# Kernel optimization log

Hardware: AMD Instinct MI355X
Metric: run time of the kernel (lower is better)

Reference implementation:

```python
import jax, jax.numpy as jnp
import numpy as np

D_MODEL = 256
D_EDGE = 64
EPS = 1e-05
INPUT_FEATS = 2 * D_MODEL + D_EDGE + 1  # 577


def _linear_params(key, fan_in, fan_out):
    k1, k2 = jax.random.split(key)
    lim = 1.0 / np.sqrt(fan_in)
    W = jax.random.uniform(k1, (fan_in, fan_out), minval=-lim, maxval=lim, dtype=jnp.float32)
    b = jax.random.uniform(k2, (fan_out,), minval=-lim, maxval=lim, dtype=jnp.float32)
    return W, b


def setup_inputs() -> dict:
    key = jax.random.key(0)
    ks = jax.random.split(key, 16)
    B, N = 8, 128
    inp = {
        "coords": jax.random.normal(ks[0], (B, N, 3), dtype=jnp.float32),
        "inv_feats": jax.random.normal(ks[1], (B, N, D_MODEL), dtype=jnp.float32),
        "adj_matrix": jnp.ones((B, N, N), dtype=jnp.float32),
        "atom_mask": jnp.ones((B, N), dtype=jnp.float32),
        "edge_feats": jax.random.normal(ks[2], (B, N, N, D_EDGE), dtype=jnp.float32),
    }
    inp["W_e1"], inp["b_e1"] = _linear_params(ks[3], INPUT_FEATS, D_MODEL)
    inp["W_e2"], inp["b_e2"] = _linear_params(ks[4], D_MODEL, D_MODEL)
    inp["W_att"], inp["b_att"] = _linear_params(ks[5], D_MODEL, 1)
    inp["W_h1"], inp["b_h1"] = _linear_params(ks[6], 2 * D_MODEL, D_MODEL)
    inp["W_h2"], inp["b_h2"] = _linear_params(ks[7], D_MODEL, D_MODEL)
    inp["W_x1"], inp["b_x1"] = _linear_params(ks[8], INPUT_FEATS, D_MODEL)
    inp["W_x2"], inp["b_x2"] = _linear_params(ks[9], D_MODEL, D_MODEL)
    inp["W_x3"], inp["b_x3"] = _linear_params(ks[10], D_MODEL, 1)
    return inp


def _pair_linear(W, b, node_feats, ef):
    # Linear over concat([node_i, node_j, ef]) without materializing the concat.
    # W: [2*d_model + d_edge + 1, out]
    d = D_MODEL
    hi = node_feats @ W[:d]          # [B,N,out]
    hj = node_feats @ W[d:2 * d]     # [B,N,out]
    he = ef @ W[2 * d:]              # [B,N,N,out]
    return hi[:, :, None, :] + hj[:, None, :, :] + he + b


def _egnn_forward(coords, inv_feats, adj_matrix, atom_mask, edge_feats,
                  W_e1, b_e1, W_e2, b_e2, W_att, b_att,
                  W_h1, b_h1, W_h2, b_h2, W_x1, b_x1, W_x2, b_x2, W_x3, b_x3):
    mask = atom_mask[..., None]                       # [B,N,1]
    diff = coords[:, :, None, :] - coords[:, None, :, :]   # [B,N,N,3]
    sq = jnp.sum(diff * diff, axis=-1, keepdims=True)      # [B,N,N,1]
    ef = jnp.concatenate([edge_feats, sq], axis=-1)        # [B,N,N,d_edge+1]
    adj = adj_matrix[..., None]                             # [B,N,N,1]

    # phi_e: Linear-SiLU-Linear-SiLU on pair features
    msg = jax.nn.silu(_pair_linear(W_e1, b_e1, inv_feats, ef))
    msg = jax.nn.silu(msg @ W_e2 + b_e2)                    # [B,N,N,d]

    att = jax.nn.sigmoid(msg @ W_att + b_att)               # [B,N,N,1]
    node_msg = jnp.sum(msg * att * adj, axis=2)             # [B,N,d]

    h = jnp.concatenate([inv_feats, node_msg], axis=-1)
    h = jax.nn.silu(h @ W_h1 + b_h1) @ W_h2 + b_h2          # [B,N,d]

    # phi_x: Linear-SiLU-Linear-SiLU-Linear -> scalar per edge
    ex = jax.nn.silu(_pair_linear(W_x1, b_x1, inv_feats, ef))
    ex = jax.nn.silu(ex @ W_x2 + b_x2)
    edge_attn = ex @ W_x3 + b_x3                             # [B,N,N,1]

    normalisers = jnp.sqrt(sq[..., 0] + EPS) + 1.0           # [B,N,N]
    weighted = diff * edge_attn / normalisers[..., None] * adj
    coord_updates = jnp.sum(weighted, axis=2)                # [B,N,3]
    num_nodes = jnp.sum(mask, axis=1) + 1.0                  # [B,1]
    coord_updates = coord_updates / num_nodes[:, :, None]

    out_coords = (coords + coord_updates) * mask
    out_feats = h * mask
    return out_coords, out_feats


def reference(coords, inv_feats, adj_matrix, atom_mask, edge_feats,
              W_e1, b_e1, W_e2, b_e2, W_att, b_att,
              W_h1, b_h1, W_h2, b_h2, W_x1, b_x1, W_x2, b_x2, W_x3, b_x3):
    return _egnn_forward(coords, inv_feats, adj_matrix, atom_mask, edge_feats,
                         W_e1, b_e1, W_e2, b_e2, W_att, b_att,
                         W_h1, b_h1, W_h2, b_h2, W_x1, b_x1, W_x2, b_x2, W_x3, b_x3)
```

## Files before the change

kernel.cpp:

```cpp
#include <hip/hip_runtime.h>

typedef __attribute__((ext_vector_type(8))) __bf16 bf16x8;
typedef __attribute__((ext_vector_type(4))) __bf16 bf16x4;
typedef __attribute__((ext_vector_type(4))) float f32x4;

__device__ __forceinline__ float fast_sig(float x) {
  return __builtin_amdgcn_rcpf(1.0f + __expf(-x));
}
__device__ __forceinline__ float siluf(float x) { return x * fast_sig(x); }
__device__ __forceinline__ __bf16 tobf(float x) { return (__bf16)x; }

__global__ __launch_bounds__(256) void k_prep(
    const float* __restrict__ We1, const float* __restrict__ Wx1,
    const float* __restrict__ We2, const float* __restrict__ Wx2,
    const float* __restrict__ Wh1, const float* __restrict__ Wh2,
    const float* __restrict__ invf,
    __bf16* __restrict__ wt_e, __bf16* __restrict__ wt_x,
    __bf16* __restrict__ w2e, __bf16* __restrict__ w2x,
    __bf16* __restrict__ wh1t, __bf16* __restrict__ wh2t,
    __bf16* __restrict__ invb,
    float* __restrict__ nmsg, float* __restrict__ cupd)
{
  int idx = blockIdx.x * 256 + threadIdx.x;
  if (idx < 147456) {
    int kk = idx / 576, f = idx - kk * 576;
    wt_e[idx] = tobf(We1[f * 256 + kk]);
    wt_x[idx] = tobf(Wx1[f * 256 + kk]);
  }
  if (idx < 65536) {
    int c = idx >> 8, k = idx & 255;
    w2e[idx] = tobf(We2[k * 256 + c]);
    w2x[idx] = tobf(Wx2[k * 256 + c]);
    wh2t[idx] = tobf(Wh2[k * 256 + c]);
    f32x4 z = {0.f, 0.f, 0.f, 0.f};
    *(f32x4*)(nmsg + idx * 4) = z;
  }
  if (idx < 131072) {
    int c = idx >> 9, k = idx & 511;
    wh1t[idx] = tobf(Wh1[k * 256 + c]);
  }
  if (idx < 3072) cupd[idx] = 0.f;
  invb[idx] = tobf(invf[idx]);
}

template<int NKS>
__device__ __forceinline__ void node_gemm64(
    const __bf16* __restrict__ B, int ldb, int boff,
    const __bf16* __restrict__ A, int lda, int aoff,
    int row0, int tid, f32x4 acc[4][4])
{
  const int lane = tid & 63, wc = tid >> 6, lr = lane & 15, lg = lane >> 4;
  #pragma unroll
  for (int ks = 0; ks < NKS; ks++) {
    bf16x8 bB[4], aA[4];
    #pragma unroll
    for (int m = 0; m < 4; m++)
      bB[m] = *(const bf16x8*)(B + (size_t)(row0 + m * 16 + lr) * ldb + boff + ks * 32 + lg * 8);
    #pragma unroll
    for (int n = 0; n < 4; n++)
      aA[n] = *(const bf16x8*)(A + (size_t)(wc * 64 + n * 16 + lr) * lda + aoff + ks * 32 + lg * 8);
    #pragma unroll
    for (int m = 0; m < 4; m++)
      #pragma unroll
      for (int n = 0; n < 4; n++)
        acc[m][n] = __builtin_amdgcn_mfma_f32_16x16x32_bf16(aA[n], bB[m], acc[m][n], 0, 0, 0);
  }
}

__global__ __launch_bounds__(256) void k_nproj(
    const __bf16* __restrict__ invb,
    const __bf16* __restrict__ wt_e, const __bf16* __restrict__ wt_x,
    const float* __restrict__ be1, const float* __restrict__ bx1,
    float* __restrict__ hie, float* __restrict__ hix,
    __bf16* __restrict__ hje, __bf16* __restrict__ hjx)
{
  const int tid = threadIdx.x;
  const int row0 = blockIdx.x * 64;
  const int mat = blockIdx.y;
  const __bf16* A = (mat < 2) ? wt_e : wt_x;
  const int aoff = (mat & 1) ? 256 : 0;

  f32x4 acc[4][4];
  #pragma unroll
  for (int m = 0; m < 4; m++)
    #pragma unroll
    for (int n = 0; n < 4; n++) { f32x4 z = {0.f,0.f,0.f,0.f}; acc[m][n] = z; }
  node_gemm64<8>(invb, 256, 0, A, 576, aoff, row0, tid, acc);

  const int lane = tid & 63, wc = tid >> 6, lr = lane & 15, lg = lane >> 4;
  if ((mat & 1) == 0) {
    const float* bias = (mat == 0) ? be1 : bx1;
    float* out = (mat == 0) ? hie : hix;
    #pragma unroll
    for (int m = 0; m < 4; m++) {
      int node = row0 + m * 16 + lr;
      #pragma unroll
      for (int n = 0; n < 4; n++) {
        int c0 = wc * 64 + n * 16 + lg * 4;
        f32x4 v = acc[m][n] + *(const f32x4*)(bias + c0);
        *(f32x4*)(out + (size_t)node * 256 + c0) = v;
      }
    }
  } else {
    __bf16* out = (mat == 1) ? hje : hjx;
    #pragma unroll
    for (int m = 0; m < 4; m++) {
      int node = row0 + m * 16 + lr;
      #pragma unroll
      for (int n = 0; n < 4; n++) {
        int c0 = wc * 64 + n * 16 + lg * 4;
        bf16x4 pk;
        #pragma unroll
        for (int r = 0; r < 4; r++) pk[r] = tobf(acc[m][n][r]);
        *(bf16x4*)(out + (size_t)node * 256 + c0) = pk;
      }
    }
  }
}

__global__ __launch_bounds__(256) void k_h1(
    const __bf16* __restrict__ invb, const float* __restrict__ nmsg,
    const __bf16* __restrict__ wh1t,
    const float* __restrict__ bh1, __bf16* __restrict__ h1b)
{
  const int tid = threadIdx.x;
  const int row0 = blockIdx.x * 64;
  const int c0 = blockIdx.y * 64;
  const int lane = tid & 63, w = tid >> 6, lr = lane & 15, lg = lane >> 4;
  const int node = row0 + w * 16 + lr;

  f32x4 acc[4];
  #pragma unroll
  for (int n = 0; n < 4; n++) { f32x4 z = {0.f,0.f,0.f,0.f}; acc[n] = z; }

  #pragma unroll
  for (int ks = 0; ks < 16; ks++) {
    bf16x8 bB;
    if (ks < 8) {
      bB = *(const bf16x8*)(invb + (size_t)node * 256 + ks * 32 + lg * 8);
    } else {
      const float* pp = nmsg + (size_t)node * 256 + (ks - 8) * 32 + lg * 8;
      f32x4 lo = *(const f32x4*)pp;
      f32x4 hi = *(const f32x4*)(pp + 4);
      bf16x8 t;
      t[0]=tobf(lo[0]); t[1]=tobf(lo[1]); t[2]=tobf(lo[2]); t[3]=tobf(lo[3]);
      t[4]=tobf(hi[0]); t[5]=tobf(hi[1]); t[6]=tobf(hi[2]); t[7]=tobf(hi[3]);
      bB = t;
    }
    #pragma unroll
    for (int n = 0; n < 4; n++) {
      bf16x8 aA = *(const bf16x8*)(wh1t + (size_t)(c0 + n * 16 + lr) * 512 + ks * 32 + lg * 8);
      acc[n] = __builtin_amdgcn_mfma_f32_16x16x32_bf16(aA, bB, acc[n], 0, 0, 0);
    }
  }

  #pragma unroll
  for (int n = 0; n < 4; n++) {
    int cc = c0 + n * 16 + lg * 4;
    f32x4 b4 = *(const f32x4*)(bh1 + cc);
    bf16x4 pk;
    #pragma unroll
    for (int r = 0; r < 4; r++) pk[r] = tobf(siluf(acc[n][r] + b4[r]));
    *(bf16x4*)(h1b + (size_t)node * 256 + cc) = pk;
  }
}

__global__ __launch_bounds__(256) void k_h2(
    const __bf16* __restrict__ h1b, const __bf16* __restrict__ wh2t,
    const float* __restrict__ bh2, const float* __restrict__ amask,
    const float* __restrict__ coords, const float* __restrict__ cupd,
    float* __restrict__ out_feats, float* __restrict__ out_coords)
{
  __shared__ float sM[2];
  const int tid = threadIdx.x;
  const int row0 = blockIdx.x * 64;
  const int c0 = blockIdx.y * 64;
  const int b = row0 >> 7;
  const int lane = tid & 63, w = tid >> 6, lr = lane & 15, lg = lane >> 4;
  const int node = row0 + w * 16 + lr;

  f32x4 acc[4];
  #pragma unroll
  for (int n = 0; n < 4; n++) { f32x4 z = {0.f,0.f,0.f,0.f}; acc[n] = z; }

  #pragma unroll
  for (int ks = 0; ks < 8; ks++) {
    bf16x8 bB = *(const bf16x8*)(h1b + (size_t)node * 256 + ks * 32 + lg * 8);
    #pragma unroll
    for (int n = 0; n < 4; n++) {
      bf16x8 aA = *(const bf16x8*)(wh2t + (size_t)(c0 + n * 16 + lr) * 256 + ks * 32 + lg * 8);
      acc[n] = __builtin_amdgcn_mfma_f32_16x16x32_bf16(aA, bB, acc[n], 0, 0, 0);
    }
  }

  float msk = amask[node];
  #pragma unroll
  for (int n = 0; n < 4; n++) {
    int cc = c0 + n * 16 + lg * 4;
    f32x4 b4 = *(const f32x4*)(bh2 + cc);
    f32x4 v = (acc[n] + b4) * msk;
    *(f32x4*)(out_feats + (size_t)node * 256 + cc) = v;
  }

  if (blockIdx.y == 0) {
    if (tid < 128) {
      float v = amask[b * 128 + tid];
      #pragma unroll
      for (int off = 1; off < 64; off <<= 1) v += __shfl_xor(v, off);
      if ((tid & 63) == 0) sM[tid >> 6] = v;
    }
    __syncthreads();
    const float sNum = sM[0] + sM[1];
    if (tid < 192) {
      int nl = tid / 3, d = tid - nl * 3;
      int nd = row0 + nl;
      float upd = cupd[nd * 3 + d] / (sNum + 1.0f);
      out_coords[nd * 3 + d] = (coords[nd * 3 + d] + upd) * amask[nd];
    }
  }
}

__global__ __launch_bounds__(512, 2) void k_edge(
    const float* __restrict__ coords, const float* __restrict__ adjm,
    const float* __restrict__ ef,
    const float* __restrict__ We1, const float* __restrict__ Wx1,
    const float* __restrict__ batt,
    const float* __restrict__ be2, const float* __restrict__ bx2,
    const float* __restrict__ bx3,
    const float* __restrict__ Watt, const float* __restrict__ Wx3,
    const float* __restrict__ hie, const float* __restrict__ hix,
    const __bf16* __restrict__ hje, const __bf16* __restrict__ hjx,
    const __bf16* __restrict__ wt_e, const __bf16* __restrict__ wt_x,
    const __bf16* __restrict__ w2e, const __bf16* __restrict__ w2x,
    float* __restrict__ nmsg, float* __restrict__ cupd)
{
  __shared__ __align__(16) char sSb[64 * 512];
  __shared__ __align__(16) __bf16 sE[2][64 * 72];
  __shared__ float sqv[2][64], sAdj[2][64], sRed[2][64];

  const int tid = threadIdx.x;
  const int d = blockIdx.x;
  const int p = (d >> 3) & 1;
  const int widx = (d >> 4) * 8 + (d & 7);
  const int lane = tid & 63;
  const int wv = tid >> 6;
  const int lr = lane & 15, lg = lane >> 4;
  const int cg = wv * 32;

  const float* hi_mat = p ? hix : hie;
  const __bf16* hj_mat = p ? hjx : hje;
  const float b0 = p ? bx3[0] : batt[0];

  f32x4 bb[2], vv[2], sl[2];
  #pragma unroll
  for (int n = 0; n < 2; n++) {
    bb[n] = *(const f32x4*)((p ? bx2 : be2) + cg + n * 16 + lg * 4);
    vv[n] = *(const f32x4*)((p ? Wx3 : Watt) + cg + n * 16 + lg * 4);
    sl[n] = *(const f32x4*)(((p ? Wx1 : We1) + 576 * 256) + cg + n * 16 + lg * 4);
  }

  const __bf16* wt = p ? wt_x : wt_e;
  const __bf16* w2 = p ? w2x : w2e;
  bf16x8 aW1[2][2], aW2[8][2];
  #pragma unroll
  for (int ks = 0; ks < 2; ks++)
    #pragma unroll
    for (int n = 0; n < 2; n++)
      aW1[ks][n] = *(const bf16x8*)(wt + (size_t)(cg + n * 16 + lr) * 576 + 512 + ks * 32 + lg * 8);
  #pragma unroll
  for (int ks = 0; ks < 8; ks++)
    #pragma unroll
    for (int n = 0; n < 2; n++)
      aW2[ks][n] = *(const bf16x8*)(w2 + (size_t)(cg + n * 16 + lr) * 256 + ks * 32 + lg * 8);

  const int erow = tid >> 3;
  const int ecol = (tid & 7) * 8;

  {
    const int h = widx * 8;
    const int bi0 = h >> 1;
    const int jg00 = (bi0 >> 7) * 128;
    if (tid < 64) {
      sRed[0][tid] = 0.f;
      int jg = jg00 + tid;
      float dx = coords[bi0 * 3 + 0] - coords[jg * 3 + 0];
      float dy = coords[bi0 * 3 + 1] - coords[jg * 3 + 1];
      float dz = coords[bi0 * 3 + 2] - coords[jg * 3 + 2];
      sqv[0][tid] = dx * dx + dy * dy + dz * dz;
    } else if (tid < 128) {
      sAdj[0][tid - 64] = adjm[(size_t)bi0 * 128 + (tid - 64)];
    }
    const float* er = ef + (size_t)bi0 * 8192 + erow * 64 + ecol;
    f32x4 x = *(const f32x4*)er;
    f32x4 y = *(const f32x4*)(er + 4);
    bf16x8 e8;
    e8[0]=tobf(x[0]); e8[1]=tobf(x[1]); e8[2]=tobf(x[2]); e8[3]=tobf(x[3]);
    e8[4]=tobf(y[0]); e8[5]=tobf(y[1]); e8[6]=tobf(y[2]); e8[7]=tobf(y[3]);
    *(bf16x8*)(&sE[0][0] + erow * 72 + ecol) = e8;
  }
  __syncthreads();

  for (int t = 0; t < 8; ++t) {
    const int h = widx * 8 + t;
    const int bi = h >> 1;
    const int jg0 = (bi >> 7) * 128 + (h & 1) * 64;
    const int cur = t & 1;
    const __bf16* sEc = &sE[cur][0];

    f32x4 hi4[2];
    bf16x4 hj4[4][2];
    #pragma unroll
    for (int n = 0; n < 2; n++)
      hi4[n] = *(const f32x4*)(hi_mat + (size_t)bi * 256 + cg + n * 16 + lg * 4);
    #pragma unroll
    for (int m = 0; m < 4; m++)
      #pragma unroll
      for (int n = 0; n < 2; n++)
        hj4[m][n] = *(const bf16x4*)(hj_mat + (size_t)(jg0 + m * 16 + lr) * 256 + cg + n * 16 + lg * 4);

    f32x4 acc[4][2];
    #pragma unroll
    for (int m = 0; m < 4; m++)
      #pragma unroll
      for (int n = 0; n < 2; n++) { f32x4 z = {0.f,0.f,0.f,0.f}; acc[m][n] = z; }

    #pragma unroll
    for (int ks = 0; ks < 2; ks++) {
      bf16x8 bE[4];
      #pragma unroll
      for (int m = 0; m < 4; m++)
        bE[m] = *(const bf16x8*)(sEc + (m * 16 + lr) * 72 + ks * 32 + lg * 8);
      __builtin_amdgcn_s_setprio(1);
      #pragma unroll
      for (int m = 0; m < 4; m++)
        #pragma unroll
        for (int n = 0; n < 2; n++)
          acc[m][n] = __builtin_amdgcn_mfma_f32_16x16x32_bf16(aW1[ks][n], bE[m], acc[m][n], 0, 0, 0);
      __builtin_amdgcn_s_setprio(0);
    }

    #pragma unroll
    for (int m = 0; m < 4; m++) {
      const int jl = m * 16 + lr;
      const float sq = sqv[cur][jl];
      #pragma unroll
      for (int n = 0; n < 2; n++) {
        const int kk0 = cg + n * 16 + lg * 4;
        bf16x4 pk;
        #pragma unroll
        for (int r = 0; r < 4; r++) {
          float v = acc[m][n][r] + hi4[n][r] + (float)hj4[m][n][r] + sq * sl[n][r];
          pk[r] = tobf(siluf(v));
        }
        int off = (jl * 512 + kk0 * 2) ^ ((jl & 7) << 4);
        *(bf16x4*)(sSb + off) = pk;
        f32x4 z = {0.f, 0.f, 0.f, 0.f};
        acc[m][n] = z;
      }
    }
    __syncthreads();

    f32x4 ex, ey;
    float nx = 0.f, ny = 0.f, nz = 0.f, njx = 0.f, njy = 0.f, njz = 0.f, nadj = 0.f;
    int bi_n = 0, jg0_n = 0;
    if (t < 7) {
      const int hn = h + 1;
      bi_n = hn >> 1;
      jg0_n = (bi_n >> 7) * 128 + (hn & 1) * 64;
      const float* er = ef + ((size_t)bi_n * 128 + (hn & 1) * 64) * 64 + erow * 64 + ecol;
      ex = *(const f32x4*)er;
      ey = *(const f32x4*)(er + 4);
      if (tid < 64) {
        int jg = jg0_n + tid;
        nx = coords[bi_n * 3 + 0]; ny = coords[bi_n * 3 + 1]; nz = coords[bi_n * 3 + 2];
        njx = coords[jg * 3 + 0]; njy = coords[jg * 3 + 1]; njz = coords[jg * 3 + 2];
      } else if (tid < 128) {
        nadj = adjm[(size_t)bi_n * 128 + ((hn & 1) * 64) + (tid - 64)];
      }
    }

    #pragma unroll
    for (int ks = 0; ks < 8; ks++) {
      bf16x8 bS[4];
      #pragma unroll
      for (int m = 0; m < 4; m++) {
        const int jl = m * 16 + lr;
        int off = (jl * 512 + (ks * 32 + lg * 8) * 2) ^ ((jl & 7) << 4);
        bS[m] = *(const bf16x8*)(sSb + off);
      }
      __builtin_amdgcn_s_setprio(1);
      #pragma unroll
      for (int m = 0; m < 4; m++)
        #pragma unroll
        for (int n = 0; n < 2; n++)
          acc[m][n] = __builtin_amdgcn_mfma_f32_16x16x32_bf16(aW2[ks][n], bS[m], acc[m][n], 0, 0, 0);
      __builtin_amdgcn_s_setprio(0);
    }

    float pr[4] = {0.f, 0.f, 0.f, 0.f};
    #pragma unroll
    for (int n = 0; n < 2; n++) {
      #pragma unroll
      for (int m = 0; m < 4; m++)
        #pragma unroll
        for (int r = 0; r < 4; r++) {
          float s = siluf(acc[m][n][r] + bb[n][r]);
          acc[m][n][r] = s;
          pr[m] += s * vv[n][r];
        }
    }
    #pragma unroll
    for (int m = 0; m < 4; m++) {
      pr[m] += __shfl_xor(pr[m], 16);
      pr[m] += __shfl_xor(pr[m], 32);
    }
    if (lane < 16) {
      #pragma unroll
      for (int m = 0; m < 4; m++)
        atomicAdd(&sRed[cur][m * 16 + lr], pr[m]);
    }

    if (t < 7) {
      const int nxt = cur ^ 1;
      bf16x8 e8;
      e8[0]=tobf(ex[0]); e8[1]=tobf(ex[1]); e8[2]=tobf(ex[2]); e8[3]=tobf(ex[3]);
      e8[4]=tobf(ey[0]); e8[5]=tobf(ey[1]); e8[6]=tobf(ey[2]); e8[7]=tobf(ey[3]);
      *(bf16x8*)(&sE[nxt][0] + erow * 72 + ecol) = e8;
      if (tid < 64) {
        sRed[nxt][tid] = 0.f;
        float dx = nx - njx, dy = ny - njy, dz = nz - njz;
        sqv[nxt][tid] = dx * dx + dy * dy + dz * dz;
      } else if (tid < 128) {
        sAdj[nxt][tid - 64] = nadj;
      }
    }
    __syncthreads();

    if (p == 0) {
      float aw[4];
      #pragma unroll
      for (int m = 0; m < 4; m++)
        aw[m] = fast_sig(sRed[cur][m * 16 + lr] + b0) * sAdj[cur][m * 16 + lr];
      f32x4 q[2];
      #pragma unroll
      for (int n = 0; n < 2; n++) { f32x4 z = {0.f,0.f,0.f,0.f}; q[n] = z; }
      #pragma unroll
      for (int m = 0; m < 4; m++)
        #pragma unroll
        for (int n = 0; n < 2; n++)
          q[n] += acc[m][n] * aw[m];
      #pragma unroll
      for (int off = 1; off < 16; off <<= 1)
        #pragma unroll
        for (int n = 0; n < 2; n++)
          #pragma unroll
          for (int r = 0; r < 4; r++)
            q[n][r] += __shfl_xor(q[n][r], off);
      if (lr == 0) {
        #pragma unroll
        for (int n = 0; n < 2; n++)
          #pragma unroll
          for (int r = 0; r < 4; r++)
            atomicAdd(&nmsg[(size_t)bi * 256 + cg + n * 16 + lg * 4 + r], q[n][r]);
      }
    } else {
      if (tid < 64) {
        int jl = tid;
        int jgl = jg0 + jl;
        float ea = sRed[cur][jl] + b0;
        float wgt = ea * __builtin_amdgcn_rcpf(sqrtf(sqv[cur][jl] + 1e-5f) + 1.0f) * sAdj[cur][jl];
        float wx = wgt * (coords[bi * 3 + 0] - coords[jgl * 3 + 0]);
        float wy = wgt * (coords[bi * 3 + 1] - coords[jgl * 3 + 1]);
        float wz = wgt * (coords[bi * 3 + 2] - coords[jgl * 3 + 2]);
        #pragma unroll
        for (int off = 1; off < 64; off <<= 1) {
          wx += __shfl_xor(wx, off);
          wy += __shfl_xor(wy, off);
          wz += __shfl_xor(wz, off);
        }
        if (tid == 0) {
          atomicAdd(&cupd[bi * 3 + 0], wx);
          atomicAdd(&cupd[bi * 3 + 1], wy);
          atomicAdd(&cupd[bi * 3 + 2], wz);
        }
      }
    }
  }
}

extern "C" void kernel_launch(void* const* d_in, const int* in_sizes, int n_in,
                              void* d_out, int out_size, void* d_ws, size_t ws_size,
                              hipStream_t stream)
{
  const float* coords = (const float*)d_in[0];
  const float* invf  = (const float*)d_in[1];
  const float* adjm  = (const float*)d_in[2];
  const float* amask = (const float*)d_in[3];
  const float* ef    = (const float*)d_in[4];
  const float* We1   = (const float*)d_in[5];
  const float* be1   = (const float*)d_in[6];
  const float* We2   = (const float*)d_in[7];
  const float* be2   = (const float*)d_in[8];
  const float* Watt  = (const float*)d_in[9];
  const float* batt  = (const float*)d_in[10];
  const float* Wh1   = (const float*)d_in[11];
  const float* bh1   = (const float*)d_in[12];
  const float* Wh2   = (const float*)d_in[13];
  const float* bh2   = (const float*)d_in[14];
  const float* Wx1   = (const float*)d_in[15];
  const float* bx1   = (const float*)d_in[16];
  const float* Wx2   = (const float*)d_in[17];
  const float* bx2   = (const float*)d_in[18];
  const float* Wx3   = (const float*)d_in[19];
  const float* bx3   = (const float*)d_in[20];

  char* ws = (char*)d_ws;
  const size_t MB = 1u << 20;
  float*  hie  = (float*)(ws + 0 * MB);
  float*  hix  = (float*)(ws + 1 * MB);
  __bf16* hje  = (__bf16*)(ws + 2 * MB);
  __bf16* hjx  = (__bf16*)(ws + 2 * MB + 524288);
  __bf16* invb = (__bf16*)(ws + 3 * MB);
  __bf16* h1b  = (__bf16*)(ws + 3 * MB + 524288);
  size_t woff = 4 * MB;
  __bf16* wt_e = (__bf16*)(ws + woff);
  __bf16* wt_x = (__bf16*)(ws + woff + 294912);
  __bf16* w2e  = (__bf16*)(ws + woff + 2 * 294912);
  __bf16* w2x  = (__bf16*)(ws + woff + 2 * 294912 + 131072);
  __bf16* wh1t = (__bf16*)(ws + woff + 2 * 294912 + 2 * 131072);
  __bf16* wh2t = (__bf16*)(ws + woff + 2 * 294912 + 2 * 131072 + 262144);
  float*  nmsg = (float*)(ws + 5 * MB + 524288);
  float*  cupd = (float*)(ws + 6 * MB + 524288);

  float* out_coords = (float*)d_out;
  float* out_feats  = out_coords + 8 * 128 * 3;

  hipLaunchKernelGGL(k_prep, dim3(1024), dim3(256), 0, stream,
                     We1, Wx1, We2, Wx2, Wh1, Wh2, invf,
                     wt_e, wt_x, w2e, w2x, wh1t, wh2t, invb, nmsg, cupd);
  hipLaunchKernelGGL(k_nproj, dim3(16, 4), dim3(256), 0, stream,
                     invb, wt_e, wt_x, be1, bx1, hie, hix, hje, hjx);
  hipLaunchKernelGGL(k_edge, dim3(512), dim3(512), 0, stream,
                     coords, adjm, ef, We1, Wx1, batt, be2, bx2, bx3, Watt, Wx3,
                     hie, hix, hje, hjx, wt_e, wt_x, w2e, w2x, nmsg, cupd);
  hipLaunchKernelGGL(k_h1, dim3(16, 4), dim3(256), 0, stream,
                     invb, nmsg, wh1t, bh1, h1b);
  hipLaunchKernelGGL(k_h2, dim3(16, 4), dim3(256), 0, stream,
                     h1b, wh2t, bh2, amask, coords, cupd, out_feats, out_coords);
}
```

Before: 150.3 us.

## Double k_edge block size so each wave owns 16 output columns

```diff
diff --git a/kernel.cpp b/kernel.cpp
--- a/kernel.cpp
+++ b/kernel.cpp
@@ -220,7 +220,7 @@
   }
 }
 
-__global__ __launch_bounds__(512, 2) void k_edge(
+__global__ __launch_bounds__(1024, 4) void k_edge(
     const float* __restrict__ coords, const float* __restrict__ adjm,
     const float* __restrict__ ef,
     const float* __restrict__ We1, const float* __restrict__ Wx1,
@@ -245,36 +245,28 @@
   const int lane = tid & 63;
   const int wv = tid >> 6;
   const int lr = lane & 15, lg = lane >> 4;
-  const int cg = wv * 32;
+  const int cg = wv * 16;
 
   const float* hi_mat = p ? hix : hie;
   const __bf16* hj_mat = p ? hjx : hje;
   const float b0 = p ? bx3[0] : batt[0];
 
-  f32x4 bb[2], vv[2], sl[2];
-  #pragma unroll
-  for (int n = 0; n < 2; n++) {
-    bb[n] = *(const f32x4*)((p ? bx2 : be2) + cg + n * 16 + lg * 4);
-    vv[n] = *(const f32x4*)((p ? Wx3 : Watt) + cg + n * 16 + lg * 4);
-    sl[n] = *(const f32x4*)(((p ? Wx1 : We1) + 576 * 256) + cg + n * 16 + lg * 4);
-  }
+  f32x4 bb = *(const f32x4*)((p ? bx2 : be2) + cg + lg * 4);
+  f32x4 vv = *(const f32x4*)((p ? Wx3 : Watt) + cg + lg * 4);
+  f32x4 sl = *(const f32x4*)(((p ? Wx1 : We1) + 576 * 256) + cg + lg * 4);
 
   const __bf16* wt = p ? wt_x : wt_e;
   const __bf16* w2 = p ? w2x : w2e;
-  bf16x8 aW1[2][2], aW2[8][2];
+  bf16x8 aW1[2], aW2[8];
   #pragma unroll
   for (int ks = 0; ks < 2; ks++)
-    #pragma unroll
-    for (int n = 0; n < 2; n++)
-      aW1[ks][n] = *(const bf16x8*)(wt + (size_t)(cg + n * 16 + lr) * 576 + 512 + ks * 32 + lg * 8);
+    aW1[ks] = *(const bf16x8*)(wt + (size_t)(cg + lr) * 576 + 512 + ks * 32 + lg * 8);
   #pragma unroll
   for (int ks = 0; ks < 8; ks++)
-    #pragma unroll
-    for (int n = 0; n < 2; n++)
-      aW2[ks][n] = *(const bf16x8*)(w2 + (size_t)(cg + n * 16 + lr) * 256 + ks * 32 + lg * 8);
-
-  const int erow = tid >> 3;
-  const int ecol = (tid & 7) * 8;
+    aW2[ks] = *(const bf16x8*)(w2 + (size_t)(cg + lr) * 256 + ks * 32 + lg * 8);
+
+  const int erow = tid >> 4;
+  const int ecol = (tid & 15) * 4;
 
   {
     const int h = widx * 8;
@@ -292,11 +284,9 @@
     }
     const float* er = ef + (size_t)bi0 * 8192 + erow * 64 + ecol;
     f32x4 x = *(const f32x4*)er;
-    f32x4 y = *(const f32x4*)(er + 4);
-    bf16x8 e8;
-    e8[0]=tobf(x[0]); e8[1]=tobf(x[1]); e8[2]=tobf(x[2]); e8[3]=tobf(x[3]);
-    e8[4]=tobf(y[0]); e8[5]=tobf(y[1]); e8[6]=tobf(y[2]); e8[7]=tobf(y[3]);
-    *(bf16x8*)(&sE[0][0] + erow * 72 + ecol) = e8;
+    bf16x4 e4;
+    e4[0]=tobf(x[0]); e4[1]=tobf(x[1]); e4[2]=tobf(x[2]); e4[3]=tobf(x[3]);
+    *(bf16x4*)(&sE[0][0] + erow * 72 + ecol) = e4;
   }
   __syncthreads();
 
@@ -307,22 +297,15 @@
     const int cur = t & 1;
     const __bf16* sEc = &sE[cur][0];
 
-    f32x4 hi4[2];
-    bf16x4 hj4[4][2];
-    #pragma unroll
-    for (int n = 0; n < 2; n++)
-      hi4[n] = *(const f32x4*)(hi_mat + (size_t)bi * 256 + cg + n * 16 + lg * 4);
+    f32x4 hi4 = *(const f32x4*)(hi_mat + (size_t)bi * 256 + cg + lg * 4);
+    bf16x4 hj4[4];
     #pragma unroll
     for (int m = 0; m < 4; m++)
-      #pragma unroll
-      for (int n = 0; n < 2; n++)
-        hj4[m][n] = *(const bf16x4*)(hj_mat + (size_t)(jg0 + m * 16 + lr) * 256 + cg + n * 16 + lg * 4);
-
-    f32x4 acc[4][2];
-    #pragma unroll
-    for (int m = 0; m < 4; m++)
-      #pragma unroll
-      for (int n = 0; n < 2; n++) { f32x4 z = {0.f,0.f,0.f,0.f}; acc[m][n] = z; }
+      hj4[m] = *(const bf16x4*)(hj_mat + (size_t)(jg0 + m * 16 + lr) * 256 + cg + lg * 4);
+
+    f32x4 acc[4];
+    #pragma unroll
+    for (int m = 0; m < 4; m++) { f32x4 z = {0.f,0.f,0.f,0.f}; acc[m] = z; }
 
     #pragma unroll
     for (int ks = 0; ks < 2; ks++) {
@@ -333,9 +316,7 @@
       __builtin_amdgcn_s_setprio(1);
       #pragma unroll
       for (int m = 0; m < 4; m++)
-        #pragma unroll
-        for (int n = 0; n < 2; n++)
-          acc[m][n] = __builtin_amdgcn_mfma_f32_16x16x32_bf16(aW1[ks][n], bE[m], acc[m][n], 0, 0, 0);
+        acc[m] = __builtin_amdgcn_mfma_f32_16x16x32_bf16(aW1[ks], bE[m], acc[m], 0, 0, 0);
       __builtin_amdgcn_s_setprio(0);
     }
 
@@ -343,33 +324,28 @@
     for (int m = 0; m < 4; m++) {
       const int jl = m * 16 + lr;
       const float sq = sqv[cur][jl];
-      #pragma unroll
-      for (int n = 0; n < 2; n++) {
-        const int kk0 = cg + n * 16 + lg * 4;
-        bf16x4 pk;
-        #pragma unroll
-        for (int r = 0; r < 4; r++) {
-          float v = acc[m][n][r] + hi4[n][r] + (float)hj4[m][n][r] + sq * sl[n][r];
-          pk[r] = tobf(siluf(v));
-        }
-        int off = (jl * 512 + kk0 * 2) ^ ((jl & 7) << 4);
-        *(bf16x4*)(sSb + off) = pk;
-        f32x4 z = {0.f, 0.f, 0.f, 0.f};
-        acc[m][n] = z;
-      }
+      const int kk0 = cg + lg * 4;
+      bf16x4 pk;
+      #pragma unroll
+      for (int r = 0; r < 4; r++) {
+        float v = acc[m][r] + hi4[r] + (float)hj4[m][r] + sq * sl[r];
+        pk[r] = tobf(siluf(v));
+      }
+      int off = (jl * 512 + kk0 * 2) ^ ((jl & 7) << 4);
+      *(bf16x4*)(sSb + off) = pk;
+      f32x4 z = {0.f, 0.f, 0.f, 0.f};
+      acc[m] = z;
     }
     __syncthreads();
 
-    f32x4 ex, ey;
+    f32x4 ex;
     float nx = 0.f, ny = 0.f, nz = 0.f, njx = 0.f, njy = 0.f, njz = 0.f, nadj = 0.f;
-    int bi_n = 0, jg0_n = 0;
     if (t < 7) {
       const int hn = h + 1;
-      bi_n = hn >> 1;
-      jg0_n = (bi_n >> 7) * 128 + (hn & 1) * 64;
+      const int bi_n = hn >> 1;
+      const int jg0_n = (bi_n >> 7) * 128 + (hn & 1) * 64;
       const float* er = ef + ((size_t)bi_n * 128 + (hn & 1) * 64) * 64 + erow * 64 + ecol;
       ex = *(const f32x4*)er;
-      ey = *(const f32x4*)(er + 4);
       if (tid < 64) {
         int jg = jg0_n + tid;
         nx = coords[bi_n * 3 + 0]; ny = coords[bi_n * 3 + 1]; nz = coords[bi_n * 3 + 2];
@@ -391,26 +367,20 @@
       __builtin_amdgcn_s_setprio(1);
       #pragma unroll
       for (int m = 0; m < 4; m++)
-        #pragma unroll
-        for (int n = 0; n < 2; n++)
-          acc[m][n] = __builtin_amdgcn_mfma_f32_16x16x32_bf16(aW2[ks][n], bS[m], acc[m][n], 0, 0, 0);
+        acc[m] = __builtin_amdgcn_mfma_f32_16x16x32_bf16(aW2[ks], bS[m], acc[m], 0, 0, 0);
       __builtin_amdgcn_s_setprio(0);
     }
 
-    float pr[4] = {0.f, 0.f, 0.f, 0.f};
-    #pragma unroll
-    for (int n = 0; n < 2; n++) {
-      #pragma unroll
-      for (int m = 0; m < 4; m++)
-        #pragma unroll
-        for (int r = 0; r < 4; r++) {
-          float s = siluf(acc[m][n][r] + bb[n][r]);
-          acc[m][n][r] = s;
-          pr[m] += s * vv[n][r];
-        }
-    }
+    float pr[4];
     #pragma unroll
     for (int m = 0; m < 4; m++) {
+      pr[m] = 0.f;
+      #pragma unroll
+      for (int r = 0; r < 4; r++) {
+        float s = siluf(acc[m][r] + bb[r]);
+        acc[m][r] = s;
+        pr[m] += s * vv[r];
+      }
       pr[m] += __shfl_xor(pr[m], 16);
       pr[m] += __shfl_xor(pr[m], 32);
     }
@@ -422,10 +392,9 @@
 
     if (t < 7) {
       const int nxt = cur ^ 1;
-      bf16x8 e8;
-      e8[0]=tobf(ex[0]); e8[1]=tobf(ex[1]); e8[2]=tobf(ex[2]); e8[3]=tobf(ex[3]);
-      e8[4]=tobf(ey[0]); e8[5]=tobf(ey[1]); e8[6]=tobf(ey[2]); e8[7]=tobf(ey[3]);
-      *(bf16x8*)(&sE[nxt][0] + erow * 72 + ecol) = e8;
+      bf16x4 e4;
+      e4[0]=tobf(ex[0]); e4[1]=tobf(ex[1]); e4[2]=tobf(ex[2]); e4[3]=tobf(ex[3]);
+      *(bf16x4*)(&sE[nxt][0] + erow * 72 + ecol) = e4;
       if (tid < 64) {
         sRed[nxt][tid] = 0.f;
         float dx = nx - njx, dy = ny - njy, dz = nz - njz;
@@ -441,27 +410,19 @@
       #pragma unroll
       for (int m = 0; m < 4; m++)
         aw[m] = fast_sig(sRed[cur][m * 16 + lr] + b0) * sAdj[cur][m * 16 + lr];
-      f32x4 q[2];
-      #pragma unroll
-      for (int n = 0; n < 2; n++) { f32x4 z = {0.f,0.f,0.f,0.f}; q[n] = z; }
+      f32x4 q = {0.f, 0.f, 0.f, 0.f};
       #pragma unroll
       for (int m = 0; m < 4; m++)
-        #pragma unroll
-        for (int n = 0; n < 2; n++)
-          q[n] += acc[m][n] * aw[m];
+        q += acc[m] * aw[m];
       #pragma unroll
       for (int off = 1; off < 16; off <<= 1)
         #pragma unroll
-        for (int n = 0; n < 2; n++)
-          #pragma unroll
-          for (int r = 0; r < 4; r++)
-            q[n][r] += __shfl_xor(q[n][r], off);
+        for (int r = 0; r < 4; r++)
+          q[r] += __shfl_xor(q[r], off);
       if (lr == 0) {
         #pragma unroll
-        for (int n = 0; n < 2; n++)
-          #pragma unroll
-          for (int r = 0; r < 4; r++)
-            atomicAdd(&nmsg[(size_t)bi * 256 + cg + n * 16 + lg * 4 + r], q[n][r]);
+        for (int r = 0; r < 4; r++)
+          atomicAdd(&nmsg[(size_t)bi * 256 + cg + lg * 4 + r], q[r]);
       }
     } else {
       if (tid < 64) {
@@ -540,7 +501,7 @@
                      wt_e, wt_x, w2e, w2x, wh1t, wh2t, invb, nmsg, cupd);
   hipLaunchKernelGGL(k_nproj, dim3(16, 4), dim3(256), 0, stream,
                      invb, wt_e, wt_x, be1, bx1, hie, hix, hje, hjx);
-  hipLaunchKernelGGL(k_edge, dim3(512), dim3(512), 0, stream,
+  hipLaunchKernelGGL(k_edge, dim3(512), dim3(1024), 0, stream,
                      coords, adjm, ef, We1, Wx1, batt, be2, bx2, bx3, Watt, Wx3,
                      hie, hix, hje, hjx, wt_e, wt_x, w2e, w2x, nmsg, cupd);
   hipLaunchKernelGGL(k_h1, dim3(16, 4), dim3(256), 0, stream,
```

Measured after the change: 267.5 us. 78.0% more time.
